# Kernel optimization log

Measured on AMD Instinct MI355X. Metric: run time of the kernel, lower is better.

The kernel has to match this reference:

```python
import jax, jax.numpy as jnp
import numpy as np
import math

EMBED_DIM = 256
KV_IN_DIM = 64
NUM_HEADS = 1
HEAD_DIM = EMBED_DIM // NUM_HEADS
ROPE_THETA = 10000.0


def rope_angles(end_x, end_y, dim, theta):
    # matches compute_axial_cis: axial (x,y) rotary angles, [end_x*end_y, dim//2]
    n = dim // 4
    f = 1.0 / (theta ** (np.arange(0, dim, 4)[:n].astype(np.float64) / dim))
    t = np.arange(end_x * end_y)
    tx = (t % end_x).astype(np.float64)
    ty = (t // end_x).astype(np.float64)
    ang = np.concatenate([np.outer(tx, f), np.outer(ty, f)], axis=-1)
    return (jnp.asarray(np.cos(ang), dtype=jnp.float32),
            jnp.asarray(np.sin(ang), dtype=jnp.float32))


def apply_rope(x, cos, sin):
    # x: [B,H,S,D]; cos/sin: [S,D//2]; complex rotation in real arithmetic
    xs = x.reshape(*x.shape[:-1], -1, 2)
    x0, x1 = xs[..., 0], xs[..., 1]
    o0 = x0 * cos - x1 * sin
    o1 = x0 * sin + x1 * cos
    return jnp.stack([o0, o1], axis=-1).reshape(x.shape)


def setup_inputs() -> dict:
    key = jax.random.key(0)
    ks = jax.random.split(key, 12)
    B, SQ, SK = 2, 4096, 16448
    q = jax.random.normal(ks[0], (B, SQ, EMBED_DIM), dtype=jnp.float32)
    k = jax.random.normal(ks[1], (B, SK, KV_IN_DIM), dtype=jnp.float32)
    v = jax.random.normal(ks[2], (B, SK, KV_IN_DIM), dtype=jnp.float32)
    attn_mask = jax.random.randint(ks[3], (B, SK, 1), 0, 2) > 0
    s_q = 1.0 / math.sqrt(EMBED_DIM)
    s_kv = 1.0 / math.sqrt(KV_IN_DIM)
    wq = jax.random.uniform(ks[4], (EMBED_DIM, EMBED_DIM), jnp.float32, -s_q, s_q)
    bq = jax.random.uniform(ks[5], (EMBED_DIM,), jnp.float32, -s_q, s_q)
    wk = jax.random.uniform(ks[6], (KV_IN_DIM, EMBED_DIM), jnp.float32, -s_kv, s_kv)
    bk = jax.random.uniform(ks[7], (EMBED_DIM,), jnp.float32, -s_kv, s_kv)
    wv = jax.random.uniform(ks[8], (KV_IN_DIM, EMBED_DIM), jnp.float32, -s_kv, s_kv)
    bv = jax.random.uniform(ks[9], (EMBED_DIM,), jnp.float32, -s_kv, s_kv)
    wo = jax.random.uniform(ks[10], (EMBED_DIM, EMBED_DIM), jnp.float32, -s_q, s_q)
    bo = jax.random.uniform(ks[11], (EMBED_DIM,), jnp.float32, -s_q, s_q)
    return {"q": q, "k": k, "v": v, "attn_mask": attn_mask,
            "wq": wq, "bq": bq, "wk": wk, "bk": bk, "wv": wv, "bv": bv,
            "wo": wo, "bo": bo, "num_k_exclude_rope": 64}


def reference(q, k, v, attn_mask, wq, bq, wk, bk, wv, bv, wo, bo, num_k_exclude_rope):
    B, SQ, _ = q.shape
    SK = k.shape[1]
    H, D = NUM_HEADS, HEAD_DIM
    # projections
    qh = (q @ wq + bq).reshape(B, SQ, H, D).transpose(0, 2, 1, 3)  # [B,H,SQ,D]
    kh = (k @ wk + bk).reshape(B, SK, H, D).transpose(0, 2, 1, 3)
    vh = (v @ wv + bv).reshape(B, SK, H, D).transpose(0, 2, 1, 3)
    # rotary encoding
    w = int(math.sqrt(SQ))
    cos, sin = rope_angles(w, w, D, ROPE_THETA)  # [SQ, D//2]
    qh = apply_rope(qh, cos, sin)
    num_k_rope = SK - num_k_exclude_rope
    r = num_k_rope // SQ  # rope_k_repeat: tile freqs over memory frames
    cos_k = jnp.tile(cos, (r, 1))
    sin_k = jnp.tile(sin, (r, 1))
    k_rot = apply_rope(kh[:, :, :num_k_rope], cos_k, sin_k)
    kh = jnp.concatenate([k_rot, kh[:, :, num_k_rope:]], axis=2)
    # masked SDPA; mask True = attend
    m = attn_mask[..., 0][:, None, None, :]  # [B,1,1,SK]
    scale = 1.0 / math.sqrt(D)
    scores = jnp.einsum("bhqd,bhkd->bhqk", qh, kh) * scale
    scores = jnp.where(m, scores, -jnp.inf)
    attn = jax.nn.softmax(scores, axis=-1)
    out = jnp.einsum("bhqk,bhkd->bhqd", attn, vh)
    out = out.transpose(0, 2, 1, 3).reshape(B, SQ, H * D)
    return out @ wo + bo
```

## Files before the change

kernel.cpp:

```cpp
#include <hip/hip_runtime.h>
#include <hip/hip_bf16.h>
#include <stdint.h>


typedef __attribute__((ext_vector_type(8))) short short8;
typedef __attribute__((ext_vector_type(4))) float f4;

__device__ __forceinline__ unsigned short f2bf(float x) {
  union { float f; uint32_t u; } v; v.f = x;
  return (unsigned short)((v.u + 0x7FFFu + ((v.u >> 16) & 1u)) >> 16);
}

__device__ __forceinline__ uint32_t cvtpk(float a, float b) {
  uint32_t r;
  asm("v_cvt_pk_bf16_f32 %0, %1, %2" : "=v"(r) : "v"(a), "v"(b));
  return r;
}

__device__ __forceinline__ void gl_lds16(const void* g, void* l) {
  __builtin_amdgcn_global_load_lds(
      (const __attribute__((address_space(1))) void*)g,
      (__attribute__((address_space(3))) void*)l, 16, 0, 0);
}

__global__ void rope_tab_k(float2* __restrict__ tab) {
  int idx = blockIdx.x * 256 + threadIdx.x;
  int t = idx >> 6, f = idx & 63;
  float freq = __expf(-(float)f * (9.210340371976184f / 64.0f));
  float ang = (float)t * freq;
  tab[idx] = make_float2(cosf(ang), sinf(ang));
}

__global__ void mask_detect_k(const unsigned int* __restrict__ m, int* __restrict__ flag) {
  __shared__ int sI, sF;
  int t = threadIdx.x;
  if (t == 0) { sI = 1; sF = 1; }
  __syncthreads();
  int okI = 1, okF = 1;
  for (int i = t; i < 2048; i += 256) {
    unsigned int w = m[i];
    if (w > 1u) okI = 0;
    if (w != 0u && w != 0x3F800000u) okF = 0;
  }
  if (!okI) atomicAnd(&sI, 0);
  if (!okF) atomicAnd(&sF, 0);
  __syncthreads();
  if (t == 0) flag[0] = sI ? 0 : (sF ? 1 : 2);
}

__device__ __forceinline__ int mask_at(const void* mk, int f, int i) {
  if (f == 0) return ((const int*)mk)[i] != 0;
  if (f == 1) return ((const float*)mk)[i] != 0.0f;
  return ((const unsigned char*)mk)[i] != 0;
}

__global__ void scan_k(const void* __restrict__ mk, const int* __restrict__ flag,
                       int* __restrict__ comp, int* __restrict__ ncomp) {
  __shared__ int sc[256];
  const int b = blockIdx.x, t = threadIdx.x, f = flag[0];
  const int base = b * 16448;
  const int c0 = t * 65, c1 = min(c0 + 65, 16448);
  int c = 0;
  for (int i = c0; i < c1; ++i) c += mask_at(mk, f, base + i);
  sc[t] = c;
  __syncthreads();
  for (int off = 1; off < 256; off <<= 1) {
    int v = (t >= off) ? sc[t - off] : 0;
    __syncthreads();
    sc[t] += v;
    __syncthreads();
  }
  int w = sc[t] - c;
  int* cb = comp + base;
  for (int i = c0; i < c1; ++i)
    if (mask_at(mk, f, base + i)) cb[w++] = i;
  if (t == 255) ncomp[b] = sc[255];
}

__global__ __launch_bounds__(256) void qproj_k(
    const float* __restrict__ q, const float* __restrict__ wq,
    const float* __restrict__ bq, const float2* __restrict__ tab,
    unsigned short* __restrict__ qh) {
  const int c = threadIdx.x;
  const int rb = blockIdx.x * 8;
  float acc[8];
  const float bias = bq[c];
#pragma unroll
  for (int r = 0; r < 8; ++r) acc[r] = bias;
  for (int ch = 0; ch < 4; ++ch) {
    float wreg[64];
#pragma unroll
    for (int j = 0; j < 64; ++j) wreg[j] = wq[(ch * 64 + j) * 256 + c];
#pragma unroll
    for (int r = 0; r < 8; ++r) {
      const float* qr = q + (size_t)(rb + r) * 256 + ch * 64;
      float a = acc[r];
#pragma unroll
      for (int j = 0; j < 64; ++j) a += qr[j] * wreg[j];
      acc[r] = a;
    }
  }
  const int p = c >> 1;
#pragma unroll
  for (int r = 0; r < 8; ++r) {
    int pos = (rb + r) & 4095;
    float2 cs = (p < 64) ? tab[(pos & 63) * 64 + p] : tab[(pos >> 6) * 64 + (p - 64)];
    float v = acc[r];
    float o = __shfl_xor(v, 1);
    float res = v * cs.x + ((c & 1) ? o * cs.y : -o * cs.y);
    qh[(size_t)(rb + r) * 256 + c] = f2bf(res * 0.0625f);
  }
}

__global__ __launch_bounds__(256) void kvproj_k(
    const float* __restrict__ kin, const float* __restrict__ vin,
    const float* __restrict__ wk, const float* __restrict__ bk,
    const float* __restrict__ wv, const float* __restrict__ bv,
    const float2* __restrict__ tab, const int* __restrict__ nker,
    const int* __restrict__ comp, const int* __restrict__ ncomp,
    unsigned short* __restrict__ kh, unsigned short* __restrict__ vt) {
  __shared__ unsigned short vlds[64 * 258];
  const int c = threadIdx.x;
  const int kb = blockIdx.x, b = blockIdx.y, kind = blockIdx.z;
  const int nc = ncomp[b];
  const int pad = (nc + 31) & ~31;
  if (kb * 64 >= pad) return;
  const float* wm = kind ? wv : wk;
  const float bias = (kind ? bv : bk)[c];
  float wreg[64];
#pragma unroll
  for (int j = 0; j < 64; ++j) wreg[j] = wm[j * 256 + c];
  const int nrope = 16448 - nker[0];
  const int* cmp = comp + b * 16448;
  const float* inb = (kind ? vin : kin) + (size_t)b * 16448 * 64;
  const int rmax = min(64, pad - kb * 64);
  for (int r = 0; r < rmax; ++r) {
    const int ci = kb * 64 + r;
    float a = 0.f;
    int oldrow = 0;
    if (ci < nc) {
      oldrow = cmp[ci];
      const float* row = inb + (size_t)oldrow * 64;
      a = bias;
#pragma unroll
      for (int j = 0; j < 64; ++j) a += row[j] * wreg[j];
    }
    if (kind == 0) {
      if (ci < nc && oldrow < nrope) {
        const int pos = oldrow & 4095, p = c >> 1;
        const float2 cs = (p < 64) ? tab[(pos & 63) * 64 + p]
                                   : tab[(pos >> 6) * 64 + (p - 64)];
        const float o = __shfl_xor(a, 1);
        a = a * cs.x + ((c & 1) ? o * cs.y : -o * cs.y);
      }
      const int kk = ci & 31;
      const int rr = ((kk >> 2) & 1) * 16 + (kk >> 3) * 4 + (kk & 3);
      const size_t rowg = (size_t)(ci & ~31) + rr;
      *(unsigned short*)((char*)kh + ((size_t)b * 16448 + rowg) * 512 +
                         ((2 * c) ^ ((rr & 7) << 4))) = f2bf(a);
    } else {
      vlds[r * 258 + c] = f2bf(a);
    }
  }
  if (kind == 1) {
    __syncthreads();
    char* tb = (char*)vt + ((size_t)b * 514 + (size_t)kb * 2) * 16384;
#pragma unroll
    for (int ti = 0; ti < 2; ++ti) {
      union { uint32_t w[16]; uint4 v4[4]; } u;
#pragma unroll
      for (int kk = 0; kk < 32; kk += 2) {
        uint32_t lo = vlds[(ti * 32 + kk) * 258 + c];
        uint32_t hi = vlds[(ti * 32 + kk + 1) * 258 + c];
        u.w[kk >> 1] = lo | (hi << 16);
      }
#pragma unroll
      for (int qd = 0; qd < 4; ++qd)
        *(uint4*)(tb + (size_t)ti * 16384 + c * 64 + qd * 16) = u.v4[qd];
    }
  }
}

__global__ __launch_bounds__(256, 3) void attn_k(
    const unsigned short* __restrict__ qh, const unsigned short* __restrict__ kh,
    const unsigned short* __restrict__ vt, const int* __restrict__ ncomp,
    float* __restrict__ part, int nseg) {
  __shared__ __align__(16) char lds[32768];
  const int tid = threadIdx.x;
  const int w = tid >> 6, ln = tid & 63;
  const int lr = ln & 15, lg = ln >> 4;
  const int segb = blockIdx.x;
  const int qb = blockIdx.y;
  const int seg = segb >> 1, b = segb & 1;
  const int nc = ncomp[b];
  const int ntiles = (nc + 31) >> 5;
  const int t0 = seg * ntiles / nseg;
  const int t1 = (seg + 1) * ntiles / nseg;

  short8 qf[8];
  {
    const unsigned short* qrow = qh + (size_t)(b * 4096 + qb * 64 + w * 16 + lr) * 256;
#pragma unroll
    for (int kc = 0; kc < 8; ++kc) qf[kc] = *(const short8*)(qrow + kc * 32 + lg * 8);
  }
  const f4 fz = {0.f, 0.f, 0.f, 0.f};
  f4 acc[16];
#pragma unroll
  for (int i = 0; i < 16; ++i) acc[i] = fz;
  float m_ = -1e30f, l_ = 0.f;

  const int S = (lr & 7) << 4;
  const int s6 = S & 64, Lo = (lg * 16) ^ (S & 48);
  const int baseE = lr * 512 + Lo + s6;
  const int baseO = lr * 512 + Lo + (64 - s6);
  const int baseV = 16384 + lr * 64 + lg * 16;

  const char* srcK = (const char*)kh + (size_t)b * 16448 * 512 + (size_t)t0 * 16384;
  const char* srcV = (const char*)vt + (size_t)b * 514 * 16384 + (size_t)t0 * 16384;
  const int stoff = tid * 16;

  for (int it = t0; it < t1; ++it) {
    __syncthreads();
#pragma unroll
    for (int r = 0; r < 4; ++r) {
      gl_lds16(srcK + r * 4096 + stoff, lds + r * 4096 + stoff);
      gl_lds16(srcV + r * 4096 + stoff, lds + 16384 + r * 4096 + stoff);
    }
    srcK += 16384; srcV += 16384;
    __syncthreads();
    f4 s[2] = {fz, fz};
#pragma unroll
    for (int kc = 0; kc < 8; ++kc) {
      const int base = (kc & 1) ? baseO : baseE;
      short8 k0 = *(const short8*)(lds + base + (kc >> 1) * 128);
      short8 k1 = *(const short8*)(lds + base + (kc >> 1) * 128 + 8192);
      s[0] = __builtin_amdgcn_mfma_f32_16x16x32_bf16(k0, qf[kc], s[0], 0, 0, 0);
      s[1] = __builtin_amdgcn_mfma_f32_16x16x32_bf16(k1, qf[kc], s[1], 0, 0, 0);
    }
    if (it * 32 + 32 > nc) {
#pragma unroll
      for (int nt = 0; nt < 2; ++nt)
#pragma unroll
        for (int j = 0; j < 4; ++j)
          if (it * 32 + lg * 8 + nt * 4 + j >= nc) s[nt][j] = -30000.f;
    }
    float tm = fmaxf(fmaxf(fmaxf(s[0][0], s[0][1]), fmaxf(s[0][2], s[0][3])),
                     fmaxf(fmaxf(s[1][0], s[1][1]), fmaxf(s[1][2], s[1][3])));
    tm = fmaxf(tm, __shfl_xor(tm, 16));
    tm = fmaxf(tm, __shfl_xor(tm, 32));
    if (!__all(tm <= m_ + 8.f)) {
      const float mn = fmaxf(m_, tm);
      const float scl = __expf(m_ - mn);
      m_ = mn; l_ *= scl;
#pragma unroll
      for (int dt = 0; dt < 16; ++dt)
#pragma unroll
        for (int j = 0; j < 4; ++j) acc[dt][j] *= scl;
    }
    float p[8];
    float ts = 0.f;
#pragma unroll
    for (int nt = 0; nt < 2; ++nt)
#pragma unroll
      for (int j = 0; j < 4; ++j) {
        float e = __expf(s[nt][j] - m_);
        p[nt * 4 + j] = e; ts += e;
      }
    ts += __shfl_xor(ts, 16);
    ts += __shfl_xor(ts, 32);
    l_ += ts;
    union { uint32_t u[4]; short8 v; } pk;
#pragma unroll
    for (int i = 0; i < 4; ++i) pk.u[i] = cvtpk(p[2 * i], p[2 * i + 1]);
    const short8 pf = pk.v;
#pragma unroll
    for (int dt = 0; dt < 16; ++dt) {
      short8 vf = *(const short8*)(lds + baseV + dt * 1024);
      acc[dt] = __builtin_amdgcn_mfma_f32_16x16x32_bf16(vf, pf, acc[dt], 0, 0, 0);
    }
  }
  float* pp = part + (size_t)(segb * 4096 + qb * 64 + w * 16 + lr) * 260;
#pragma unroll
  for (int dt = 0; dt < 16; ++dt) *(f4*)(pp + dt * 16 + lg * 4) = acc[dt];
  if (lg == 0) { pp[256] = m_; pp[257] = l_; }
}

__global__ void combine_k(const float* __restrict__ part, int nseg,
                          float* __restrict__ attn) {
  const int row = blockIdx.x;
  const int b = row >> 12, rl = row & 4095;
  const int d = threadIdx.x;
  float M = -1e30f;
  for (int s = 0; s < nseg; ++s)
    M = fmaxf(M, part[(size_t)((s * 2 + b) * 4096 + rl) * 260 + 256]);
  float L = 0.f, val = 0.f;
  for (int s = 0; s < nseg; ++s) {
    size_t ix = (size_t)((s * 2 + b) * 4096 + rl) * 260;
    float wf = __expf(part[ix + 256] - M);
    L += part[ix + 257] * wf;
    val += part[ix + d] * wf;
  }
  attn[(size_t)row * 256 + d] = val / L;
}

__global__ __launch_bounds__(256) void ogemm_k(
    const float* __restrict__ in, const float* __restrict__ wo,
    const float* __restrict__ bo, float* __restrict__ out) {
  const int c = threadIdx.x;
  const int rb = blockIdx.x * 8;
  float acc[8];
  const float bias = bo[c];
#pragma unroll
  for (int r = 0; r < 8; ++r) acc[r] = bias;
  for (int ch = 0; ch < 4; ++ch) {
    float wreg[64];
#pragma unroll
    for (int j = 0; j < 64; ++j) wreg[j] = wo[(ch * 64 + j) * 256 + c];
#pragma unroll
    for (int r = 0; r < 8; ++r) {
      const float* ir = in + (size_t)(rb + r) * 256 + ch * 64;
      float a = acc[r];
#pragma unroll
      for (int j = 0; j < 64; ++j) a += ir[j] * wreg[j];
      acc[r] = a;
    }
  }
#pragma unroll
  for (int r = 0; r < 8; ++r) out[(size_t)(rb + r) * 256 + c] = acc[r];
}

extern "C" void kernel_launch(void* const* d_in, const int* in_sizes, int n_in,
                              void* d_out, int out_size, void* d_ws, size_t ws_size,
                              hipStream_t stream) {
  const float* q  = (const float*)d_in[0];
  const float* k  = (const float*)d_in[1];
  const float* v  = (const float*)d_in[2];
  const void*  mk = d_in[3];
  const float* wq = (const float*)d_in[4];
  const float* bq = (const float*)d_in[5];
  const float* wk = (const float*)d_in[6];
  const float* bk = (const float*)d_in[7];
  const float* wv = (const float*)d_in[8];
  const float* bv = (const float*)d_in[9];
  const float* wo = (const float*)d_in[10];
  const float* bo = (const float*)d_in[11];
  const int* nker = (const int*)d_in[12];
  (void)in_sizes; (void)n_in; (void)out_size;

  char* ws = (char*)d_ws;
  size_t off = 0;
  auto alloc = [&](size_t sz) { size_t o = off; off = (off + sz + 255) & ~(size_t)255; return o; };
  const size_t o_tab  = alloc((size_t)64 * 64 * 8);
  const size_t o_qh   = alloc((size_t)8192 * 256 * 2);
  const size_t o_kh   = alloc((size_t)2 * 16448 * 512);
  const size_t o_vt   = alloc((size_t)2 * 514 * 16384);
  const size_t o_cmp  = alloc((size_t)2 * 16448 * 4);
  const size_t o_ncmp = alloc(256);
  const size_t o_flag = alloc(256);
  const size_t o_attn = alloc((size_t)8192 * 256 * 4);
  const size_t o_part = off;
  auto partsz = [](int s) { return (size_t)s * 2 * 4096 * 260 * 4; };
  int nseg = 8;
  while (nseg > 1 && o_part + partsz(nseg) > ws_size) nseg >>= 1;

  float2* tab        = (float2*)(ws + o_tab);
  unsigned short* qh = (unsigned short*)(ws + o_qh);
  unsigned short* kh = (unsigned short*)(ws + o_kh);
  unsigned short* vt = (unsigned short*)(ws + o_vt);
  int* comp          = (int*)(ws + o_cmp);
  int* ncomp         = (int*)(ws + o_ncmp);
  int* flag          = (int*)(ws + o_flag);
  float* attn        = (float*)(ws + o_attn);
  float* part        = (float*)(ws + o_part);

  rope_tab_k<<<dim3(16), dim3(256), 0, stream>>>(tab);
  mask_detect_k<<<dim3(1), dim3(256), 0, stream>>>((const unsigned int*)mk, flag);
  scan_k<<<dim3(2), dim3(256), 0, stream>>>(mk, flag, comp, ncomp);
  qproj_k<<<dim3(1024), dim3(256), 0, stream>>>(q, wq, bq, tab, qh);
  kvproj_k<<<dim3(257, 2, 2), dim3(256), 0, stream>>>(k, v, wk, bk, wv, bv, tab, nker,
                                                      comp, ncomp, kh, vt);
  attn_k<<<dim3(nseg * 2, 64), dim3(256), 0, stream>>>(qh, kh, vt, ncomp, part, nseg);
  combine_k<<<dim3(8192), dim3(256), 0, stream>>>(part, nseg, attn);
  ogemm_k<<<dim3(1024), dim3(256), 0, stream>>>(attn, wo, bo, (float*)d_out);
}
```

Before: 426.1 us.

## Process two query groups per wave, read V from global, fuse combine into output GEMM

The attention kernel now handles 32 query rows per wave (128 per block), so each loaded K/V fragment feeds twice as many MFMAs. V is no longer staged in LDS and is read straight from global/L2, which halves LDS use. The split-softmax combine is fused into the output projection kernel, dropping the intermediate attn buffer and one launch. In exchange, register pressure roughly doubles (occupancy hint lowered to 2), the grid halves, and V reads now depend on cache hit rates.

```diff
diff --git a/kernel.cpp b/kernel.cpp
--- a/kernel.cpp
+++ b/kernel.cpp
@@ -181,11 +181,11 @@
   }
 }
 
-__global__ __launch_bounds__(256, 3) void attn_k(
+__global__ __launch_bounds__(256, 2) void attn_k(
     const unsigned short* __restrict__ qh, const unsigned short* __restrict__ kh,
     const unsigned short* __restrict__ vt, const int* __restrict__ ncomp,
     float* __restrict__ part, int nseg) {
-  __shared__ __align__(16) char lds[32768];
+  __shared__ __align__(16) char lds[16384];
   const int tid = threadIdx.x;
   const int w = tid >> 6, ln = tid & 63;
   const int lr = ln & 15, lg = ln >> 4;
@@ -197,117 +197,144 @@
   const int t0 = seg * ntiles / nseg;
   const int t1 = (seg + 1) * ntiles / nseg;
 
-  short8 qf[8];
+  short8 qf[2][8];
   {
-    const unsigned short* qrow = qh + (size_t)(b * 4096 + qb * 64 + w * 16 + lr) * 256;
-#pragma unroll
-    for (int kc = 0; kc < 8; ++kc) qf[kc] = *(const short8*)(qrow + kc * 32 + lg * 8);
+    const unsigned short* qr = qh + (size_t)(b * 4096 + qb * 128 + w * 32 + lr) * 256;
+#pragma unroll
+    for (int g = 0; g < 2; ++g)
+#pragma unroll
+      for (int kc = 0; kc < 8; ++kc)
+        qf[g][kc] = *(const short8*)(qr + g * 16 * 256 + kc * 32 + lg * 8);
   }
   const f4 fz = {0.f, 0.f, 0.f, 0.f};
-  f4 acc[16];
-#pragma unroll
-  for (int i = 0; i < 16; ++i) acc[i] = fz;
-  float m_ = -1e30f, l_ = 0.f;
+  f4 acc[2][16];
+#pragma unroll
+  for (int g = 0; g < 2; ++g)
+#pragma unroll
+    for (int i = 0; i < 16; ++i) acc[g][i] = fz;
+  float m_[2] = {-1e30f, -1e30f}, l_[2] = {0.f, 0.f};
 
   const int S = (lr & 7) << 4;
   const int s6 = S & 64, Lo = (lg * 16) ^ (S & 48);
   const int baseE = lr * 512 + Lo + s6;
   const int baseO = lr * 512 + Lo + (64 - s6);
-  const int baseV = 16384 + lr * 64 + lg * 16;
 
   const char* srcK = (const char*)kh + (size_t)b * 16448 * 512 + (size_t)t0 * 16384;
-  const char* srcV = (const char*)vt + (size_t)b * 514 * 16384 + (size_t)t0 * 16384;
+  const char* gV = (const char*)vt + (size_t)b * 514 * 16384 + (size_t)t0 * 16384
+                   + lr * 64 + lg * 16;
   const int stoff = tid * 16;
 
   for (int it = t0; it < t1; ++it) {
     __syncthreads();
 #pragma unroll
-    for (int r = 0; r < 4; ++r) {
+    for (int r = 0; r < 4; ++r)
       gl_lds16(srcK + r * 4096 + stoff, lds + r * 4096 + stoff);
-      gl_lds16(srcV + r * 4096 + stoff, lds + 16384 + r * 4096 + stoff);
-    }
-    srcK += 16384; srcV += 16384;
+    srcK += 16384;
     __syncthreads();
-    f4 s[2] = {fz, fz};
+    f4 s[2][2] = {{fz, fz}, {fz, fz}};
 #pragma unroll
     for (int kc = 0; kc < 8; ++kc) {
-      const int base = (kc & 1) ? baseO : baseE;
-      short8 k0 = *(const short8*)(lds + base + (kc >> 1) * 128);
-      short8 k1 = *(const short8*)(lds + base + (kc >> 1) * 128 + 8192);
-      s[0] = __builtin_amdgcn_mfma_f32_16x16x32_bf16(k0, qf[kc], s[0], 0, 0, 0);
-      s[1] = __builtin_amdgcn_mfma_f32_16x16x32_bf16(k1, qf[kc], s[1], 0, 0, 0);
+      const int off = ((kc & 1) ? baseO : baseE) + (kc >> 1) * 128;
+      short8 k0 = *(const short8*)(lds + off);
+      short8 k1 = *(const short8*)(lds + off + 8192);
+      s[0][0] = __builtin_amdgcn_mfma_f32_16x16x32_bf16(k0, qf[0][kc], s[0][0], 0, 0, 0);
+      s[1][0] = __builtin_amdgcn_mfma_f32_16x16x32_bf16(k0, qf[1][kc], s[1][0], 0, 0, 0);
+      s[0][1] = __builtin_amdgcn_mfma_f32_16x16x32_bf16(k1, qf[0][kc], s[0][1], 0, 0, 0);
+      s[1][1] = __builtin_amdgcn_mfma_f32_16x16x32_bf16(k1, qf[1][kc], s[1][1], 0, 0, 0);
     }
     if (it * 32 + 32 > nc) {
 #pragma unroll
       for (int nt = 0; nt < 2; ++nt)
 #pragma unroll
         for (int j = 0; j < 4; ++j)
-          if (it * 32 + lg * 8 + nt * 4 + j >= nc) s[nt][j] = -30000.f;
-    }
-    float tm = fmaxf(fmaxf(fmaxf(s[0][0], s[0][1]), fmaxf(s[0][2], s[0][3])),
-                     fmaxf(fmaxf(s[1][0], s[1][1]), fmaxf(s[1][2], s[1][3])));
-    tm = fmaxf(tm, __shfl_xor(tm, 16));
-    tm = fmaxf(tm, __shfl_xor(tm, 32));
-    if (!__all(tm <= m_ + 8.f)) {
-      const float mn = fmaxf(m_, tm);
-      const float scl = __expf(m_ - mn);
-      m_ = mn; l_ *= scl;
-#pragma unroll
-      for (int dt = 0; dt < 16; ++dt)
-#pragma unroll
-        for (int j = 0; j < 4; ++j) acc[dt][j] *= scl;
-    }
-    float p[8];
-    float ts = 0.f;
-#pragma unroll
-    for (int nt = 0; nt < 2; ++nt)
-#pragma unroll
-      for (int j = 0; j < 4; ++j) {
-        float e = __expf(s[nt][j] - m_);
-        p[nt * 4 + j] = e; ts += e;
+          if (it * 32 + lg * 8 + nt * 4 + j >= nc) {
+            s[0][nt][j] = -30000.f; s[1][nt][j] = -30000.f;
+          }
+    }
+    float tm[2];
+#pragma unroll
+    for (int g = 0; g < 2; ++g) {
+      float t = fmaxf(fmaxf(fmaxf(s[g][0][0], s[g][0][1]), fmaxf(s[g][0][2], s[g][0][3])),
+                      fmaxf(fmaxf(s[g][1][0], s[g][1][1]), fmaxf(s[g][1][2], s[g][1][3])));
+      t = fmaxf(t, __shfl_xor(t, 16));
+      t = fmaxf(t, __shfl_xor(t, 32));
+      tm[g] = t;
+    }
+    if (!__all(tm[0] <= m_[0] + 8.f && tm[1] <= m_[1] + 8.f)) {
+#pragma unroll
+      for (int g = 0; g < 2; ++g) {
+        const float mn = fmaxf(m_[g], tm[g]);
+        const float sc = __expf(m_[g] - mn);
+        m_[g] = mn; l_[g] *= sc;
+#pragma unroll
+        for (int dt = 0; dt < 16; ++dt)
+#pragma unroll
+          for (int j = 0; j < 4; ++j) acc[g][dt][j] *= sc;
       }
-    ts += __shfl_xor(ts, 16);
-    ts += __shfl_xor(ts, 32);
-    l_ += ts;
-    union { uint32_t u[4]; short8 v; } pk;
-#pragma unroll
-    for (int i = 0; i < 4; ++i) pk.u[i] = cvtpk(p[2 * i], p[2 * i + 1]);
-    const short8 pf = pk.v;
-#pragma unroll
-    for (int dt = 0; dt < 16; ++dt) {
-      short8 vf = *(const short8*)(lds + baseV + dt * 1024);
-      acc[dt] = __builtin_amdgcn_mfma_f32_16x16x32_bf16(vf, pf, acc[dt], 0, 0, 0);
-    }
-  }
-  float* pp = part + (size_t)(segb * 4096 + qb * 64 + w * 16 + lr) * 260;
-#pragma unroll
-  for (int dt = 0; dt < 16; ++dt) *(f4*)(pp + dt * 16 + lg * 4) = acc[dt];
-  if (lg == 0) { pp[256] = m_; pp[257] = l_; }
-}
-
-__global__ void combine_k(const float* __restrict__ part, int nseg,
-                          float* __restrict__ attn) {
-  const int row = blockIdx.x;
-  const int b = row >> 12, rl = row & 4095;
-  const int d = threadIdx.x;
-  float M = -1e30f;
-  for (int s = 0; s < nseg; ++s)
-    M = fmaxf(M, part[(size_t)((s * 2 + b) * 4096 + rl) * 260 + 256]);
-  float L = 0.f, val = 0.f;
-  for (int s = 0; s < nseg; ++s) {
-    size_t ix = (size_t)((s * 2 + b) * 4096 + rl) * 260;
-    float wf = __expf(part[ix + 256] - M);
-    L += part[ix + 257] * wf;
-    val += part[ix + d] * wf;
-  }
-  attn[(size_t)row * 256 + d] = val / L;
-}
-
-__global__ __launch_bounds__(256) void ogemm_k(
-    const float* __restrict__ in, const float* __restrict__ wo,
+    }
+    short8 pf[2];
+#pragma unroll
+    for (int g = 0; g < 2; ++g) {
+      union { uint32_t u[4]; short8 v; } pk;
+      float ts = 0.f;
+#pragma unroll
+      for (int nt = 0; nt < 2; ++nt)
+#pragma unroll
+        for (int jj = 0; jj < 4; jj += 2) {
+          float e0 = __expf(s[g][nt][jj] - m_[g]);
+          float e1 = __expf(s[g][nt][jj + 1] - m_[g]);
+          ts += e0 + e1;
+          pk.u[nt * 2 + (jj >> 1)] = cvtpk(e0, e1);
+        }
+      ts += __shfl_xor(ts, 16);
+      ts += __shfl_xor(ts, 32);
+      l_[g] += ts;
+      pf[g] = pk.v;
+    }
+#pragma unroll
+    for (int bt = 0; bt < 4; ++bt) {
+      short8 vf[4];
+#pragma unroll
+      for (int i = 0; i < 4; ++i) vf[i] = *(const short8*)(gV + (bt * 4 + i) * 1024);
+#pragma unroll
+      for (int dt = 0; dt < 4; ++dt) {
+        acc[0][bt * 4 + dt] = __builtin_amdgcn_mfma_f32_16x16x32_bf16(vf[dt], pf[0], acc[0][bt * 4 + dt], 0, 0, 0);
+        acc[1][bt * 4 + dt] = __builtin_amdgcn_mfma_f32_16x16x32_bf16(vf[dt], pf[1], acc[1][bt * 4 + dt], 0, 0, 0);
+      }
+    }
+    gV += 16384;
+  }
+  const int qrow = qb * 128 + w * 32 + lr;
+#pragma unroll
+  for (int g = 0; g < 2; ++g) {
+    float* pp = part + ((size_t)segb * 4096 + qrow + g * 16) * 260;
+#pragma unroll
+    for (int dt = 0; dt < 16; ++dt) *(f4*)(pp + dt * 16 + lg * 4) = acc[g][dt];
+    if (lg == 0) { pp[256] = m_[g]; pp[257] = l_[g]; }
+  }
+}
+
+__global__ __launch_bounds__(256) void cogemm_k(
+    const float* __restrict__ part, int nseg, const float* __restrict__ wo,
     const float* __restrict__ bo, float* __restrict__ out) {
+  __shared__ float rows[8][256];
   const int c = threadIdx.x;
   const int rb = blockIdx.x * 8;
+  for (int r = 0; r < 8; ++r) {
+    const int row = rb + r, b = row >> 12, rl = row & 4095;
+    float M = -1e30f;
+    for (int s = 0; s < nseg; ++s)
+      M = fmaxf(M, part[(size_t)((s * 2 + b) * 4096 + rl) * 260 + 256]);
+    float L = 0.f, val = 0.f;
+    for (int s = 0; s < nseg; ++s) {
+      size_t ix = (size_t)((s * 2 + b) * 4096 + rl) * 260;
+      float wf = __expf(part[ix + 256] - M);
+      L += part[ix + 257] * wf;
+      val += part[ix + c] * wf;
+    }
+    rows[r][c] = val / L;
+  }
+  __syncthreads();
   float acc[8];
   const float bias = bo[c];
 #pragma unroll
@@ -318,7 +345,7 @@
     for (int j = 0; j < 64; ++j) wreg[j] = wo[(ch * 64 + j) * 256 + c];
 #pragma unroll
     for (int r = 0; r < 8; ++r) {
-      const float* ir = in + (size_t)(rb + r) * 256 + ch * 64;
+      const float* ir = &rows[r][ch * 64];
       float a = acc[r];
 #pragma unroll
       for (int j = 0; j < 64; ++j) a += ir[j] * wreg[j];
@@ -357,7 +384,6 @@
   const size_t o_cmp  = alloc((size_t)2 * 16448 * 4);
   const size_t o_ncmp = alloc(256);
   const size_t o_flag = alloc(256);
-  const size_t o_attn = alloc((size_t)8192 * 256 * 4);
   const size_t o_part = off;
   auto partsz = [](int s) { return (size_t)s * 2 * 4096 * 260 * 4; };
   int nseg = 8;
@@ -370,7 +396,6 @@
   int* comp          = (int*)(ws + o_cmp);
   int* ncomp         = (int*)(ws + o_ncmp);
   int* flag          = (int*)(ws + o_flag);
-  float* attn        = (float*)(ws + o_attn);
   float* part        = (float*)(ws + o_part);
 
   rope_tab_k<<<dim3(16), dim3(256), 0, stream>>>(tab);
@@ -379,7 +404,6 @@
   qproj_k<<<dim3(1024), dim3(256), 0, stream>>>(q, wq, bq, tab, qh);
   kvproj_k<<<dim3(257, 2, 2), dim3(256), 0, stream>>>(k, v, wk, bk, wv, bv, tab, nker,
                                                       comp, ncomp, kh, vt);
-  attn_k<<<dim3(nseg * 2, 64), dim3(256), 0, stream>>>(qh, kh, vt, ncomp, part, nseg);
-  combine_k<<<dim3(8192), dim3(256), 0, stream>>>(part, nseg, attn);
-  ogemm_k<<<dim3(1024), dim3(256), 0, stream>>>(attn, wo, bo, (float*)d_out);
-}
+  attn_k<<<dim3(nseg * 2, 32), dim3(256), 0, stream>>>(qh, kh, vt, ncomp, part, nseg);
+  cogemm_k<<<dim3(1024), dim3(256), 0, stream>>>(part, nseg, wo, bo, (float*)d_out);
+}
```

After: 391.1 us. 8.2% less time.
